# Performance work log

Hardware: AMD Instinct MI355X
Metric: run time of the kernel (lower is better)

Reference implementation:

```python
import jax, jax.numpy as jnp
import numpy as np

B, L, D = 8, 2048, 64
NEG = -1e9  # matches torch masked fill value -1000000000.0


def setup_inputs() -> dict:
    key = jax.random.key(0)
    kq, kk, kv = jax.random.split(key, 3)
    return {
        "q": jax.random.normal(kq, (B, L, D), dtype=jnp.float32),
        "k": jax.random.normal(kk, (B, L, D), dtype=jnp.float32),
        "v": jax.random.normal(kv, (B, L, D), dtype=jnp.float32),
    }


def reference(q, k, v):
    d_k = q.shape[-1]
    scale = 1.0 / np.sqrt(d_k).astype(np.float32)
    # [B, Lq, Lk] scores
    scores = jnp.einsum("bqd,bkd->bqk", q, k) * scale
    n = scores.shape[-1]
    i = jnp.arange(n)[:, None]
    j = jnp.arange(n)[None, :]
    # fw_mask: tril(diag=-1) of -1e9 -> strictly-lower entries penalized (attend to self+future)
    fw = scores + jnp.where(j < i, jnp.float32(NEG), jnp.float32(0.0))
    # bw_mask: triu(diag=1) of -1e9 -> strictly-upper entries penalized (attend to past+self)
    bw = scores + jnp.where(j > i, jnp.float32(NEG), jnp.float32(0.0))
    out = jnp.einsum("bqk,bkd->bqd", jax.nn.softmax(fw, axis=-1), v) \
        + jnp.einsum("bqk,bkd->bqd", jax.nn.softmax(bw, axis=-1), v)
    return out
```

## Files before the change

kernel.cpp:

```cpp
#include <hip/hip_runtime.h>


typedef __attribute__((ext_vector_type(8))) short short8;
typedef __attribute__((ext_vector_type(4))) float f32x4;

union Frag {
    short8 s;
    unsigned u[4];
    uint4 u4;
};

#define MFMA16(A, B, C) __builtin_amdgcn_mfma_f32_16x16x32_bf16((A), (B), (C), 0, 0, 0)

static constexpr int BB = 8, LL = 2048, DD = 64;
static constexpr float QSCALE = 0.125f * 1.44269504088896340736f;

__device__ __forceinline__ unsigned pk2(float a, float b) {
    unsigned ua = __builtin_bit_cast(unsigned, a) + 0x8000u;
    unsigned ub = __builtin_bit_cast(unsigned, b) + 0x8000u;
    return __builtin_amdgcn_perm(ub, ua, 0x07060302u);
}

__device__ __forceinline__ unsigned bperm(int addr, unsigned v) {
    return (unsigned)__builtin_amdgcn_ds_bpermute(addr, (int)v);
}

__global__ __launch_bounds__(256)
void prepack_frags(const float* __restrict__ K, const float* __restrict__ V,
                   unsigned* __restrict__ Kf, unsigned* __restrict__ Vf) {
    const int t    = threadIdx.x;
    const int lane = t & 63;
    const int col  = lane & 15;
    const int quad = lane >> 4;
    const int g    = t >> 6;
    if (blockIdx.x < 512) {
        const int b = blockIdx.x >> 6, jblk = blockIdx.x & 63, j0 = jblk << 5;
        const int f = g >> 1, h = g & 1;
        const float* src = K + ((size_t)(b * LL) + j0 + 16 * f + col) * DD + h * 32 + quad * 8;
        float4 a0 = *(const float4*)(src);
        float4 a1 = *(const float4*)(src + 4);
        uint4 o = make_uint4(pk2(a0.x, a0.y), pk2(a0.z, a0.w),
                             pk2(a1.x, a1.y), pk2(a1.z, a1.w));
        *(uint4*)(Kf + (size_t)(b * 64 + jblk) * 1024 + t * 4) = o;
    } else {
        const int idx = blockIdx.x - 512;
        const int b = idx >> 6, jblk = idx & 63, j0 = jblk << 5;
        const float* src = V + ((size_t)(b * LL) + j0 + quad * 8) * DD + 16 * g + col;
        float e[8];
        #pragma unroll
        for (int kk = 0; kk < 8; ++kk) e[kk] = src[(size_t)kk * DD];
        uint4 o = make_uint4(pk2(e[0], e[1]), pk2(e[2], e[3]),
                             pk2(e[4], e[5]), pk2(e[6], e[7]));
        *(uint4*)(Vf + (size_t)(b * 64 + jblk) * 1024 + t * 4) = o;
    }
}

__global__ __launch_bounds__(256, 3)
void attn_v3(const float* __restrict__ Q, const unsigned* __restrict__ Kf,
             const unsigned* __restrict__ Vf, float* __restrict__ O) {
    __shared__ __align__(16) float red[9216];

    const int tid  = threadIdx.x;
    const int w    = tid >> 6;
    const int lane = tid & 63;
    const int col  = lane & 15;
    const int quad = lane >> 4;

    const int b  = blockIdx.x & 7;
    const int i0 = (blockIdx.x >> 3) << 4;

    Frag qf[2];
    {
        const float* qr = Q + ((size_t)(b * LL) + i0 + col) * DD + quad * 8;
        float4 a0 = *(const float4*)(qr + 0);
        float4 a1 = *(const float4*)(qr + 4);
        float4 a2 = *(const float4*)(qr + 32);
        float4 a3 = *(const float4*)(qr + 36);
        qf[0].u[0] = pk2(a0.x * QSCALE, a0.y * QSCALE);
        qf[0].u[1] = pk2(a0.z * QSCALE, a0.w * QSCALE);
        qf[0].u[2] = pk2(a1.x * QSCALE, a1.y * QSCALE);
        qf[0].u[3] = pk2(a1.z * QSCALE, a1.w * QSCALE);
        qf[1].u[0] = pk2(a2.x * QSCALE, a2.y * QSCALE);
        qf[1].u[1] = pk2(a2.z * QSCALE, a2.w * QSCALE);
        qf[1].u[2] = pk2(a3.x * QSCALE, a3.y * QSCALE);
        qf[1].u[3] = pk2(a3.z * QSCALE, a3.w * QSCALE);
    }

    const int kbase = w << 9;
    const int dj0   = i0 & ~31;
    const unsigned* kp = Kf + (size_t)(b * 64 + (kbase >> 5)) * 1024 + lane * 4;
    const unsigned* vp = Vf + (size_t)(b * 64 + (kbase >> 5)) * 1024 + lane * 4;

    f32x4 zero = {0.f, 0.f, 0.f, 0.f};
    f32x4 ot[2][4];
    #pragma unroll
    for (int s = 0; s < 2; ++s)
        #pragma unroll
        for (int c = 0; c < 4; ++c) ot[s][c] = zero;
    float lsumF = 0.f, lsumB = 0.f;

    const int  bpA = (32 * (quad & 1) + col) << 2;
    const bool hiq = quad >= 2;

    Frag ka[4], vf[4], kan[4], vfn[4];
    #pragma unroll
    for (int g = 0; g < 4; ++g) {
        ka[g].u4 = *(const uint4*)(kp + g * 256);
        vf[g].u4 = *(const uint4*)(vp + g * 256);
    }

    for (int blk = 0; blk < 16; ++blk) {
        const int j0 = kbase + (blk << 5);
        const int no = ((blk + 1) & 15) << 10;
        #pragma unroll
        for (int g = 0; g < 4; ++g) {
            kan[g].u4 = *(const uint4*)(kp + no + g * 256);
            vfn[g].u4 = *(const uint4*)(vp + no + g * 256);
        }

        f32x4 st0 = zero, st1 = zero;
        st0 = MFMA16(ka[0].s, qf[0].s, st0);
        st0 = MFMA16(ka[1].s, qf[1].s, st0);
        st1 = MFMA16(ka[2].s, qf[0].s, st1);
        st1 = MFMA16(ka[3].s, qf[1].s, st1);

        float p0[4], p1[4];
        #pragma unroll
        for (int r = 0; r < 4; ++r) { p0[r] = exp2f(st0[r]); p1[r] = exp2f(st1[r]); }

        const bool mixed = (j0 == dj0);

        if (j0 >= dj0) {
            float m0[4], m1[4];
            if (mixed) {
                const int ig = i0 + col;
                #pragma unroll
                for (int r = 0; r < 4; ++r) {
                    const int jg = j0 + 4 * quad + r;
                    m0[r] = (jg >= ig) ? p0[r] : 0.f;
                    m1[r] = (jg + 16 >= ig) ? p1[r] : 0.f;
                }
            } else {
                #pragma unroll
                for (int r = 0; r < 4; ++r) { m0[r] = p0[r]; m1[r] = p1[r]; }
            }
            lsumF += m0[0] + m0[1] + m0[2] + m0[3] + m1[0] + m1[1] + m1[2] + m1[3];
            unsigned x01 = pk2(m0[0], m0[1]), x23 = pk2(m0[2], m0[3]);
            unsigned y01 = pk2(m1[0], m1[1]), y23 = pk2(m1[2], m1[3]);
            unsigned a0 = bperm(bpA, x01),      a1 = bperm(bpA, x23);
            unsigned a2 = bperm(bpA + 64, x01), a3 = bperm(bpA + 64, x23);
            unsigned b0 = bperm(bpA, y01),      b1 = bperm(bpA, y23);
            unsigned b2 = bperm(bpA + 64, y01), b3 = bperm(bpA + 64, y23);
            Frag pf;
            pf.u[0] = hiq ? b0 : a0;
            pf.u[1] = hiq ? b1 : a1;
            pf.u[2] = hiq ? b2 : a2;
            pf.u[3] = hiq ? b3 : a3;
            #pragma unroll
            for (int c = 0; c < 4; ++c) ot[0][c] = MFMA16(vf[c].s, pf.s, ot[0][c]);
        }
        if (j0 <= dj0) {
            float m0[4], m1[4];
            if (mixed) {
                const int ig = i0 + col;
                #pragma unroll
                for (int r = 0; r < 4; ++r) {
                    const int jg = j0 + 4 * quad + r;
                    m0[r] = (jg <= ig) ? p0[r] : 0.f;
                    m1[r] = (jg + 16 <= ig) ? p1[r] : 0.f;
                }
            } else {
                #pragma unroll
                for (int r = 0; r < 4; ++r) { m0[r] = p0[r]; m1[r] = p1[r]; }
            }
            lsumB += m0[0] + m0[1] + m0[2] + m0[3] + m1[0] + m1[1] + m1[2] + m1[3];
            unsigned x01 = pk2(m0[0], m0[1]), x23 = pk2(m0[2], m0[3]);
            unsigned y01 = pk2(m1[0], m1[1]), y23 = pk2(m1[2], m1[3]);
            unsigned a0 = bperm(bpA, x01),      a1 = bperm(bpA, x23);
            unsigned a2 = bperm(bpA + 64, x01), a3 = bperm(bpA + 64, x23);
            unsigned b0 = bperm(bpA, y01),      b1 = bperm(bpA, y23);
            unsigned b2 = bperm(bpA + 64, y01), b3 = bperm(bpA + 64, y23);
            Frag pg;
            pg.u[0] = hiq ? b0 : a0;
            pg.u[1] = hiq ? b1 : a1;
            pg.u[2] = hiq ? b2 : a2;
            pg.u[3] = hiq ? b3 : a3;
            #pragma unroll
            for (int c = 0; c < 4; ++c) ot[1][c] = MFMA16(vf[c].s, pg.s, ot[1][c]);
        }

        #pragma unroll
        for (int g = 0; g < 4; ++g) { ka[g] = kan[g]; vf[g] = vfn[g]; }
    }

    #pragma unroll
    for (int s = 0; s < 2; ++s)
        #pragma unroll
        for (int c = 0; c < 4; ++c)
            *(f32x4*)&red[((w * 2 + s) * 16 + col) * 68 + 16 * c + 4 * quad] = ot[s][c];
    red[8704 + ((w * 2 + 0) * 4 + quad) * 16 + col] = lsumF;
    red[8704 + ((w * 2 + 1) * 4 + quad) * 16 + col] = lsumB;
    __syncthreads();

    const int q  = tid >> 4;
    const int d0 = (tid & 15) << 2;
    float lf = 0.f, lb = 0.f;
    #pragma unroll
    for (int w2 = 0; w2 < 4; ++w2)
        #pragma unroll
        for (int qd = 0; qd < 4; ++qd) {
            lf += red[8704 + ((w2 * 2 + 0) * 4 + qd) * 16 + q];
            lb += red[8704 + ((w2 * 2 + 1) * 4 + qd) * 16 + q];
        }
    f32x4 aF = {0.f, 0.f, 0.f, 0.f}, aB = aF;
    #pragma unroll
    for (int w2 = 0; w2 < 4; ++w2) {
        aF += *(const f32x4*)&red[((w2 * 2 + 0) * 16 + q) * 68 + d0];
        aB += *(const f32x4*)&red[((w2 * 2 + 1) * 16 + q) * 68 + d0];
    }
    const float rf = 1.0f / lf;
    const float rb = 1.0f / lb;
    float4 o = {aF[0] * rf + aB[0] * rb, aF[1] * rf + aB[1] * rb,
                aF[2] * rf + aB[2] * rb, aF[3] * rf + aB[3] * rb};
    *(float4*)(O + ((size_t)(b * LL) + i0 + q) * DD + d0) = o;
}

__global__ __launch_bounds__(256)
void attn_fused_v1(const float* __restrict__ Q, const float* __restrict__ K,
                   const float* __restrict__ V, float* __restrict__ O) {
    __shared__ unsigned smem[8448];
    const int tid  = threadIdx.x;
    const int w    = tid >> 6;
    const int lane = tid & 63;
    const int col  = lane & 15;
    const int quad = lane >> 4;
    const int b  = blockIdx.x >> 7;
    const int i0 = (blockIdx.x & 127) << 4;
    const float* Qb = Q + (size_t)(b * LL + i0) * DD;
    const float* Kb = K + (size_t)b * LL * DD;
    const float* Vb = V + (size_t)b * LL * DD;
    unsigned* VT = smem + w * 1280;
    unsigned* Pb = smem + 5120 + w * 640;
    Frag qf[2];
    {
        const float* qr = Qb + col * DD + quad * 8;
        float4 a0 = *(const float4*)(qr + 0);
        float4 a1 = *(const float4*)(qr + 4);
        float4 a2 = *(const float4*)(qr + 32);
        float4 a3 = *(const float4*)(qr + 36);
        qf[0].u[0] = pk2(a0.x * QSCALE, a0.y * QSCALE);
        qf[0].u[1] = pk2(a0.z * QSCALE, a0.w * QSCALE);
        qf[0].u[2] = pk2(a1.x * QSCALE, a1.y * QSCALE);
        qf[0].u[3] = pk2(a1.z * QSCALE, a1.w * QSCALE);
        qf[1].u[0] = pk2(a2.x * QSCALE, a2.y * QSCALE);
        qf[1].u[1] = pk2(a2.z * QSCALE, a2.w * QSCALE);
        qf[1].u[2] = pk2(a3.x * QSCALE, a3.y * QSCALE);
        qf[1].u[3] = pk2(a3.z * QSCALE, a3.w * QSCALE);
    }
    Frag ones;
    ones.u[0] = ones.u[1] = ones.u[2] = ones.u[3] = 0x3F803F80u;
    f32x4 zero = {0.f, 0.f, 0.f, 0.f};
    f32x4 ot[2][4];
    f32x4 lacc[2];
    lacc[0] = zero; lacc[1] = zero;
    for (int s = 0; s < 2; ++s)
        for (int c = 0; c < 4; ++c) ot[s][c] = zero;
    const int kbase = w << 9;
    const int dj0   = i0 & ~31;
    for (int blk = 0; blk < 16; ++blk) {
        const int j0 = kbase + (blk << 5);
        Frag ka[2][2];
        for (int f = 0; f < 2; ++f) {
            const float* kr = Kb + (size_t)(j0 + f * 16 + col) * DD + quad * 8;
            float4 c0 = *(const float4*)(kr + 0);
            float4 c1 = *(const float4*)(kr + 4);
            float4 c2 = *(const float4*)(kr + 32);
            float4 c3 = *(const float4*)(kr + 36);
            ka[f][0].u[0] = pk2(c0.x, c0.y);
            ka[f][0].u[1] = pk2(c0.z, c0.w);
            ka[f][0].u[2] = pk2(c1.x, c1.y);
            ka[f][0].u[3] = pk2(c1.z, c1.w);
            ka[f][1].u[0] = pk2(c2.x, c2.y);
            ka[f][1].u[1] = pk2(c2.z, c2.w);
            ka[f][1].u[2] = pk2(c3.x, c3.y);
            ka[f][1].u[3] = pk2(c3.z, c3.w);
        }
        for (int u = 0; u < 4; ++u) {
            const int d0 = u * 16 + quad * 4;
            const float* va = Vb + (size_t)(j0 + 2 * col) * DD + d0;
            float4 x = *(const float4*)(va);
            float4 y = *(const float4*)(va + DD);
            VT[(d0 + 0) * 20 + col] = pk2(x.x, y.x);
            VT[(d0 + 1) * 20 + col] = pk2(x.y, y.y);
            VT[(d0 + 2) * 20 + col] = pk2(x.z, y.z);
            VT[(d0 + 3) * 20 + col] = pk2(x.w, y.w);
        }
        f32x4 st0 = zero, st1 = zero;
        st0 = MFMA16(ka[0][0].s, qf[0].s, st0);
        st0 = MFMA16(ka[0][1].s, qf[1].s, st0);
        st1 = MFMA16(ka[1][0].s, qf[0].s, st1);
        st1 = MFMA16(ka[1][1].s, qf[1].s, st1);
        float p0[4], p1[4];
        for (int r = 0; r < 4; ++r) { p0[r] = exp2f(st0[r]); p1[r] = exp2f(st1[r]); }
        bool doF, doB;
        if (j0 == dj0) {
            const int ig = i0 + col;
            unsigned* prowF = Pb + col * 20 + quad * 2;
            unsigned* prowB = prowF + 320;
            float m0[4], m1[4];
            for (int r = 0; r < 4; ++r) {
                const int jg = j0 + 4 * quad + r;
                m0[r] = (jg >= ig) ? p0[r] : 0.f;
                m1[r] = (jg + 16 >= ig) ? p1[r] : 0.f;
            }
            prowF[0] = pk2(m0[0], m0[1]);
            prowF[1] = pk2(m0[2], m0[3]);
            prowF[8] = pk2(m1[0], m1[1]);
            prowF[9] = pk2(m1[2], m1[3]);
            for (int r = 0; r < 4; ++r) {
                const int jg = j0 + 4 * quad + r;
                m0[r] = (jg <= ig) ? p0[r] : 0.f;
                m1[r] = (jg + 16 <= ig) ? p1[r] : 0.f;
            }
            prowB[0] = pk2(m0[0], m0[1]);
            prowB[1] = pk2(m0[2], m0[3]);
            prowB[8] = pk2(m1[0], m1[1]);
            prowB[9] = pk2(m1[2], m1[3]);
            doF = true; doB = true;
        } else if (j0 < i0) {
            unsigned* prowB = Pb + 320 + col * 20 + quad * 2;
            prowB[0] = pk2(p0[0], p0[1]);
            prowB[1] = pk2(p0[2], p0[3]);
            prowB[8] = pk2(p1[0], p1[1]);
            prowB[9] = pk2(p1[2], p1[3]);
            doF = false; doB = true;
        } else {
            unsigned* prowF = Pb + col * 20 + quad * 2;
            prowF[0] = pk2(p0[0], p0[1]);
            prowF[1] = pk2(p0[2], p0[3]);
            prowF[8] = pk2(p1[0], p1[1]);
            prowF[9] = pk2(p1[2], p1[3]);
            doF = true; doB = false;
        }
        Frag vfr[4];
        for (int c = 0; c < 4; ++c)
            vfr[c].u4 = *(const uint4*)(VT + (16 * c + col) * 20 + quad * 4);
        if (doF) {
            Frag pf; pf.u4 = *(const uint4*)(Pb + col * 20 + quad * 4);
            lacc[0] = MFMA16(ones.s, pf.s, lacc[0]);
            for (int c = 0; c < 4; ++c) ot[0][c] = MFMA16(vfr[c].s, pf.s, ot[0][c]);
        }
        if (doB) {
            Frag pg; pg.u4 = *(const uint4*)(Pb + 320 + col * 20 + quad * 4);
            lacc[1] = MFMA16(ones.s, pg.s, lacc[1]);
            for (int c = 0; c < 4; ++c) ot[1][c] = MFMA16(vfr[c].s, pg.s, ot[1][c]);
        }
    }
    __syncthreads();
    float* red  = (float*)smem;
    float* lred = (float*)(smem + 8192);
    for (int s = 0; s < 2; ++s)
        for (int c = 0; c < 4; ++c)
            for (int r = 0; r < 4; ++r)
                red[((w * 2 + s) * 64 + 16 * c + 4 * quad + r) * 16 + col] = ot[s][c][r];
    if (lane < 16) {
        lred[(w * 2 + 0) * 16 + col] = lacc[0][0];
        lred[(w * 2 + 1) * 16 + col] = lacc[1][0];
    }
    __syncthreads();
    const int ri = tid >> 4;
    const int db = (tid & 15) << 2;
    float lf = 0.f, lb = 0.f;
    for (int w2 = 0; w2 < 4; ++w2) {
        lf += lred[(w2 * 2 + 0) * 16 + ri];
        lb += lred[(w2 * 2 + 1) * 16 + ri];
    }
    const float rf = 1.0f / lf;
    const float rb = 1.0f / lb;
    float acc[4];
    for (int kk = 0; kk < 4; ++kk) {
        float af = 0.f, ab = 0.f;
        for (int w2 = 0; w2 < 4; ++w2) {
            af += red[((w2 * 2 + 0) * 64 + db + kk) * 16 + ri];
            ab += red[((w2 * 2 + 1) * 64 + db + kk) * 16 + ri];
        }
        acc[kk] = af * rf + ab * rb;
    }
    float4 o = {acc[0], acc[1], acc[2], acc[3]};
    *(float4*)(O + (size_t)(b * LL + i0 + ri) * DD + db) = o;
}

extern "C" void kernel_launch(void* const* d_in, const int* in_sizes, int n_in,
                              void* d_out, int out_size, void* d_ws, size_t ws_size,
                              hipStream_t stream) {
    const float* q = (const float*)d_in[0];
    const float* k = (const float*)d_in[1];
    const float* v = (const float*)d_in[2];
    float* o = (float*)d_out;
    (void)in_sizes; (void)n_in; (void)out_size;

    const size_t WS_NEED = (size_t)2 * BB * 64 * 1024 * 4 * sizeof(unsigned);
    if (ws_size >= WS_NEED) {
        unsigned* Kf = (unsigned*)d_ws;
        unsigned* Vf = Kf + (size_t)BB * 64 * 1024;
        prepack_frags<<<dim3(1024), dim3(256), 0, stream>>>(k, v, Kf, Vf);
        attn_v3<<<dim3(1024), dim3(256), 0, stream>>>(q, Kf, Vf, o);
    } else {
        attn_fused_v1<<<dim3(BB * (LL / 16)), dim3(256), 0, stream>>>(q, k, v, o);
    }
}
```

Measured before the change: 87.24 us.

## Process 32 query rows per block to reuse K/V fragments across two query tiles

Each block now handles two 16-row query tiles, so every loaded K and V fragment feeds twice as many MFMAs, and the grid is halved to 512 blocks. The KV loop is manually unrolled by two with ping-pong fragment buffers instead of copying next-to-current registers each iteration. The aim is to halve global K/V fragment traffic per unit of work. The cost is more registers, doubled shared memory for the reduction, launch bounds lowered to 2 blocks per SM, and fewer blocks to spread across CUs.

```diff
diff --git a/kernel.cpp b/kernel.cpp
--- a/kernel.cpp
+++ b/kernel.cpp
@@ -55,10 +55,10 @@
     }
 }
 
-__global__ __launch_bounds__(256, 3)
-void attn_v3(const float* __restrict__ Q, const unsigned* __restrict__ Kf,
+__global__ __launch_bounds__(256, 2)
+void attn_v4(const float* __restrict__ Q, const unsigned* __restrict__ Kf,
              const unsigned* __restrict__ Vf, float* __restrict__ O) {
-    __shared__ __align__(16) float red[9216];
+    __shared__ __align__(16) float red[18432];
 
     const int tid  = threadIdx.x;
     const int w    = tid >> 6;
@@ -67,162 +67,197 @@
     const int quad = lane >> 4;
 
     const int b  = blockIdx.x & 7;
-    const int i0 = (blockIdx.x >> 3) << 4;
-
-    Frag qf[2];
+    const int i0 = (blockIdx.x >> 3) << 5;
+
+    Frag qf[2][2];
     {
         const float* qr = Q + ((size_t)(b * LL) + i0 + col) * DD + quad * 8;
-        float4 a0 = *(const float4*)(qr + 0);
-        float4 a1 = *(const float4*)(qr + 4);
-        float4 a2 = *(const float4*)(qr + 32);
-        float4 a3 = *(const float4*)(qr + 36);
-        qf[0].u[0] = pk2(a0.x * QSCALE, a0.y * QSCALE);
-        qf[0].u[1] = pk2(a0.z * QSCALE, a0.w * QSCALE);
-        qf[0].u[2] = pk2(a1.x * QSCALE, a1.y * QSCALE);
-        qf[0].u[3] = pk2(a1.z * QSCALE, a1.w * QSCALE);
-        qf[1].u[0] = pk2(a2.x * QSCALE, a2.y * QSCALE);
-        qf[1].u[1] = pk2(a2.z * QSCALE, a2.w * QSCALE);
-        qf[1].u[2] = pk2(a3.x * QSCALE, a3.y * QSCALE);
-        qf[1].u[3] = pk2(a3.z * QSCALE, a3.w * QSCALE);
+        #pragma unroll
+        for (int qt = 0; qt < 2; ++qt) {
+            const float* qp = qr + (size_t)qt * 16 * DD;
+            float4 a0 = *(const float4*)(qp + 0);
+            float4 a1 = *(const float4*)(qp + 4);
+            float4 a2 = *(const float4*)(qp + 32);
+            float4 a3 = *(const float4*)(qp + 36);
+            qf[qt][0].u[0] = pk2(a0.x * QSCALE, a0.y * QSCALE);
+            qf[qt][0].u[1] = pk2(a0.z * QSCALE, a0.w * QSCALE);
+            qf[qt][0].u[2] = pk2(a1.x * QSCALE, a1.y * QSCALE);
+            qf[qt][0].u[3] = pk2(a1.z * QSCALE, a1.w * QSCALE);
+            qf[qt][1].u[0] = pk2(a2.x * QSCALE, a2.y * QSCALE);
+            qf[qt][1].u[1] = pk2(a2.z * QSCALE, a2.w * QSCALE);
+            qf[qt][1].u[2] = pk2(a3.x * QSCALE, a3.y * QSCALE);
+            qf[qt][1].u[3] = pk2(a3.z * QSCALE, a3.w * QSCALE);
+        }
     }
 
     const int kbase = w << 9;
-    const int dj0   = i0 & ~31;
     const unsigned* kp = Kf + (size_t)(b * 64 + (kbase >> 5)) * 1024 + lane * 4;
     const unsigned* vp = Vf + (size_t)(b * 64 + (kbase >> 5)) * 1024 + lane * 4;
 
     f32x4 zero = {0.f, 0.f, 0.f, 0.f};
-    f32x4 ot[2][4];
+    f32x4 ot[2][2][4];
     #pragma unroll
     for (int s = 0; s < 2; ++s)
         #pragma unroll
-        for (int c = 0; c < 4; ++c) ot[s][c] = zero;
-    float lsumF = 0.f, lsumB = 0.f;
+        for (int qt = 0; qt < 2; ++qt)
+            #pragma unroll
+            for (int c = 0; c < 4; ++c) ot[s][qt][c] = zero;
+    float lsF[2] = {0.f, 0.f}, lsB[2] = {0.f, 0.f};
 
     const int  bpA = (32 * (quad & 1) + col) << 2;
     const bool hiq = quad >= 2;
 
-    Frag ka[4], vf[4], kan[4], vfn[4];
+    Frag kaA[4], vfA[4], kaB[4], vfB[4];
     #pragma unroll
     for (int g = 0; g < 4; ++g) {
-        ka[g].u4 = *(const uint4*)(kp + g * 256);
-        vf[g].u4 = *(const uint4*)(vp + g * 256);
-    }
-
-    for (int blk = 0; blk < 16; ++blk) {
+        kaA[g].u4 = *(const uint4*)(kp + g * 256);
+        vfA[g].u4 = *(const uint4*)(vp + g * 256);
+    }
+
+    auto body = [&](Frag (&ck)[4], Frag (&cv)[4], Frag (&nk)[4], Frag (&nv)[4],
+                    const int blk) {
         const int j0 = kbase + (blk << 5);
         const int no = ((blk + 1) & 15) << 10;
         #pragma unroll
         for (int g = 0; g < 4; ++g) {
-            kan[g].u4 = *(const uint4*)(kp + no + g * 256);
-            vfn[g].u4 = *(const uint4*)(vp + no + g * 256);
-        }
-
-        f32x4 st0 = zero, st1 = zero;
-        st0 = MFMA16(ka[0].s, qf[0].s, st0);
-        st0 = MFMA16(ka[1].s, qf[1].s, st0);
-        st1 = MFMA16(ka[2].s, qf[0].s, st1);
-        st1 = MFMA16(ka[3].s, qf[1].s, st1);
-
-        float p0[4], p1[4];
-        #pragma unroll
-        for (int r = 0; r < 4; ++r) { p0[r] = exp2f(st0[r]); p1[r] = exp2f(st1[r]); }
-
-        const bool mixed = (j0 == dj0);
-
-        if (j0 >= dj0) {
-            float m0[4], m1[4];
-            if (mixed) {
-                const int ig = i0 + col;
+            nk[g].u4 = *(const uint4*)(kp + no + g * 256);
+            nv[g].u4 = *(const uint4*)(vp + no + g * 256);
+        }
+
+        f32x4 st00 = zero, st01 = zero, st10 = zero, st11 = zero;
+        st00 = MFMA16(ck[0].s, qf[0][0].s, st00);
+        st00 = MFMA16(ck[1].s, qf[0][1].s, st00);
+        st01 = MFMA16(ck[0].s, qf[1][0].s, st01);
+        st01 = MFMA16(ck[1].s, qf[1][1].s, st01);
+        st10 = MFMA16(ck[2].s, qf[0][0].s, st10);
+        st10 = MFMA16(ck[3].s, qf[0][1].s, st10);
+        st11 = MFMA16(ck[2].s, qf[1][0].s, st11);
+        st11 = MFMA16(ck[3].s, qf[1][1].s, st11);
+
+        float p0[2][4], p1[2][4];
+        #pragma unroll
+        for (int r = 0; r < 4; ++r) {
+            p0[0][r] = exp2f(st00[r]);
+            p0[1][r] = exp2f(st01[r]);
+            p1[0][r] = exp2f(st10[r]);
+            p1[1][r] = exp2f(st11[r]);
+        }
+
+        const bool mixed = (j0 == i0);
+
+        if (j0 >= i0) {
+            #pragma unroll
+            for (int qt = 0; qt < 2; ++qt) {
+                float m0[4], m1[4];
+                if (mixed) {
+                    const int ig = i0 + 16 * qt + col;
+                    #pragma unroll
+                    for (int r = 0; r < 4; ++r) {
+                        const int jg = j0 + 4 * quad + r;
+                        m0[r] = (jg >= ig) ? p0[qt][r] : 0.f;
+                        m1[r] = (jg + 16 >= ig) ? p1[qt][r] : 0.f;
+                    }
+                } else {
+                    #pragma unroll
+                    for (int r = 0; r < 4; ++r) { m0[r] = p0[qt][r]; m1[r] = p1[qt][r]; }
+                }
+                lsF[qt] += m0[0] + m0[1] + m0[2] + m0[3] + m1[0] + m1[1] + m1[2] + m1[3];
+                unsigned x01 = pk2(m0[0], m0[1]), x23 = pk2(m0[2], m0[3]);
+                unsigned y01 = pk2(m1[0], m1[1]), y23 = pk2(m1[2], m1[3]);
+                unsigned a0 = bperm(bpA, x01),      a1 = bperm(bpA, x23);
+                unsigned a2 = bperm(bpA + 64, x01), a3 = bperm(bpA + 64, x23);
+                unsigned b0 = bperm(bpA, y01),      b1 = bperm(bpA, y23);
+                unsigned b2 = bperm(bpA + 64, y01), b3 = bperm(bpA + 64, y23);
+                Frag pf;
+                pf.u[0] = hiq ? b0 : a0;
+                pf.u[1] = hiq ? b1 : a1;
+                pf.u[2] = hiq ? b2 : a2;
+                pf.u[3] = hiq ? b3 : a3;
                 #pragma unroll
-                for (int r = 0; r < 4; ++r) {
-                    const int jg = j0 + 4 * quad + r;
-                    m0[r] = (jg >= ig) ? p0[r] : 0.f;
-                    m1[r] = (jg + 16 >= ig) ? p1[r] : 0.f;
+                for (int c = 0; c < 4; ++c)
+                    ot[0][qt][c] = MFMA16(cv[c].s, pf.s, ot[0][qt][c]);
+            }
+        }
+        if (j0 <= i0) {
+            #pragma unroll
+            for (int qt = 0; qt < 2; ++qt) {
+                float m0[4], m1[4];
+                if (mixed) {
+                    const int ig = i0 + 16 * qt + col;
+                    #pragma unroll
+                    for (int r = 0; r < 4; ++r) {
+                        const int jg = j0 + 4 * quad + r;
+                        m0[r] = (jg <= ig) ? p0[qt][r] : 0.f;
+                        m1[r] = (jg + 16 <= ig) ? p1[qt][r] : 0.f;
+                    }
+                } else {
+                    #pragma unroll
+                    for (int r = 0; r < 4; ++r) { m0[r] = p0[qt][r]; m1[r] = p1[qt][r]; }
                 }
-            } else {
+                lsB[qt] += m0[0] + m0[1] + m0[2] + m0[3] + m1[0] + m1[1] + m1[2] + m1[3];
+                unsigned x01 = pk2(m0[0], m0[1]), x23 = pk2(m0[2], m0[3]);
+                unsigned y01 = pk2(m1[0], m1[1]), y23 = pk2(m1[2], m1[3]);
+                unsigned a0 = bperm(bpA, x01),      a1 = bperm(bpA, x23);
+                unsigned a2 = bperm(bpA + 64, x01), a3 = bperm(bpA + 64, x23);
+                unsigned b0 = bperm(bpA, y01),      b1 = bperm(bpA, y23);
+                unsigned b2 = bperm(bpA + 64, y01), b3 = bperm(bpA + 64, y23);
+                Frag pg;
+                pg.u[0] = hiq ? b0 : a0;
+                pg.u[1] = hiq ? b1 : a1;
+                pg.u[2] = hiq ? b2 : a2;
+                pg.u[3] = hiq ? b3 : a3;
                 #pragma unroll
-                for (int r = 0; r < 4; ++r) { m0[r] = p0[r]; m1[r] = p1[r]; }
+                for (int c = 0; c < 4; ++c)
+                    ot[1][qt][c] = MFMA16(cv[c].s, pg.s, ot[1][qt][c]);
             }
-            lsumF += m0[0] + m0[1] + m0[2] + m0[3] + m1[0] + m1[1] + m1[2] + m1[3];
-            unsigned x01 = pk2(m0[0], m0[1]), x23 = pk2(m0[2], m0[3]);
-            unsigned y01 = pk2(m1[0], m1[1]), y23 = pk2(m1[2], m1[3]);
-            unsigned a0 = bperm(bpA, x01),      a1 = bperm(bpA, x23);
-            unsigned a2 = bperm(bpA + 64, x01), a3 = bperm(bpA + 64, x23);
-            unsigned b0 = bperm(bpA, y01),      b1 = bperm(bpA, y23);
-            unsigned b2 = bperm(bpA + 64, y01), b3 = bperm(bpA + 64, y23);
-            Frag pf;
-            pf.u[0] = hiq ? b0 : a0;
-            pf.u[1] = hiq ? b1 : a1;
-            pf.u[2] = hiq ? b2 : a2;
-            pf.u[3] = hiq ? b3 : a3;
-            #pragma unroll
-            for (int c = 0; c < 4; ++c) ot[0][c] = MFMA16(vf[c].s, pf.s, ot[0][c]);
-        }
-        if (j0 <= dj0) {
-            float m0[4], m1[4];
-            if (mixed) {
-                const int ig = i0 + col;
-                #pragma unroll
-                for (int r = 0; r < 4; ++r) {
-                    const int jg = j0 + 4 * quad + r;
-                    m0[r] = (jg <= ig) ? p0[r] : 0.f;
-                    m1[r] = (jg + 16 <= ig) ? p1[r] : 0.f;
-                }
-            } else {
-                #pragma unroll
-                for (int r = 0; r < 4; ++r) { m0[r] = p0[r]; m1[r] = p1[r]; }
-            }
-            lsumB += m0[0] + m0[1] + m0[2] + m0[3] + m1[0] + m1[1] + m1[2] + m1[3];
-            unsigned x01 = pk2(m0[0], m0[1]), x23 = pk2(m0[2], m0[3]);
-            unsigned y01 = pk2(m1[0], m1[1]), y23 = pk2(m1[2], m1[3]);
-            unsigned a0 = bperm(bpA, x01),      a1 = bperm(bpA, x23);
-            unsigned a2 = bperm(bpA + 64, x01), a3 = bperm(bpA + 64, x23);
-            unsigned b0 = bperm(bpA, y01),      b1 = bperm(bpA, y23);
-            unsigned b2 = bperm(bpA + 64, y01), b3 = bperm(bpA + 64, y23);
-            Frag pg;
-            pg.u[0] = hiq ? b0 : a0;
-            pg.u[1] = hiq ? b1 : a1;
-            pg.u[2] = hiq ? b2 : a2;
-            pg.u[3] = hiq ? b3 : a3;
-            #pragma unroll
-            for (int c = 0; c < 4; ++c) ot[1][c] = MFMA16(vf[c].s, pg.s, ot[1][c]);
-        }
-
-        #pragma unroll
-        for (int g = 0; g < 4; ++g) { ka[g] = kan[g]; vf[g] = vfn[g]; }
+        }
+    };
+
+    for (int it = 0; it < 8; ++it) {
+        body(kaA, vfA, kaB, vfB, 2 * it);
+        body(kaB, vfB, kaA, vfA, 2 * it + 1);
     }
 
     #pragma unroll
     for (int s = 0; s < 2; ++s)
         #pragma unroll
-        for (int c = 0; c < 4; ++c)
-            *(f32x4*)&red[((w * 2 + s) * 16 + col) * 68 + 16 * c + 4 * quad] = ot[s][c];
-    red[8704 + ((w * 2 + 0) * 4 + quad) * 16 + col] = lsumF;
-    red[8704 + ((w * 2 + 1) * 4 + quad) * 16 + col] = lsumB;
+        for (int qt = 0; qt < 2; ++qt)
+            #pragma unroll
+            for (int c = 0; c < 4; ++c)
+                *(f32x4*)&red[((w * 2 + s) * 32 + qt * 16 + col) * 68 + 16 * c + 4 * quad] =
+                    ot[s][qt][c];
+    #pragma unroll
+    for (int qt = 0; qt < 2; ++qt) {
+        red[17408 + (((w * 2 + 0) * 2 + qt) * 4 + quad) * 16 + col] = lsF[qt];
+        red[17408 + (((w * 2 + 1) * 2 + qt) * 4 + quad) * 16 + col] = lsB[qt];
+    }
     __syncthreads();
 
     const int q  = tid >> 4;
     const int d0 = (tid & 15) << 2;
-    float lf = 0.f, lb = 0.f;
     #pragma unroll
-    for (int w2 = 0; w2 < 4; ++w2)
-        #pragma unroll
-        for (int qd = 0; qd < 4; ++qd) {
-            lf += red[8704 + ((w2 * 2 + 0) * 4 + qd) * 16 + q];
-            lb += red[8704 + ((w2 * 2 + 1) * 4 + qd) * 16 + q];
-        }
-    f32x4 aF = {0.f, 0.f, 0.f, 0.f}, aB = aF;
-    #pragma unroll
-    for (int w2 = 0; w2 < 4; ++w2) {
-        aF += *(const f32x4*)&red[((w2 * 2 + 0) * 16 + q) * 68 + d0];
-        aB += *(const f32x4*)&red[((w2 * 2 + 1) * 16 + q) * 68 + d0];
-    }
-    const float rf = 1.0f / lf;
-    const float rb = 1.0f / lb;
-    float4 o = {aF[0] * rf + aB[0] * rb, aF[1] * rf + aB[1] * rb,
-                aF[2] * rf + aB[2] * rb, aF[3] * rf + aB[3] * rb};
-    *(float4*)(O + ((size_t)(b * LL) + i0 + q) * DD + d0) = o;
+    for (int qh = 0; qh < 2; ++qh) {
+        const int qq = qh * 16 + q;
+        float lf = 0.f, lb = 0.f;
+        #pragma unroll
+        for (int w2 = 0; w2 < 4; ++w2)
+            #pragma unroll
+            for (int qd = 0; qd < 4; ++qd) {
+                lf += red[17408 + (((w2 * 2 + 0) * 2 + qh) * 4 + qd) * 16 + q];
+                lb += red[17408 + (((w2 * 2 + 1) * 2 + qh) * 4 + qd) * 16 + q];
+            }
+        f32x4 aF = {0.f, 0.f, 0.f, 0.f}, aB = aF;
+        #pragma unroll
+        for (int w2 = 0; w2 < 4; ++w2) {
+            aF += *(const f32x4*)&red[((w2 * 2 + 0) * 32 + qq) * 68 + d0];
+            aB += *(const f32x4*)&red[((w2 * 2 + 1) * 32 + qq) * 68 + d0];
+        }
+        const float rf = 1.0f / lf;
+        const float rb = 1.0f / lb;
+        float4 o = {aF[0] * rf + aB[0] * rb, aF[1] * rf + aB[1] * rb,
+                    aF[2] * rf + aB[2] * rb, aF[3] * rf + aB[3] * rb};
+        *(float4*)(O + ((size_t)(b * LL) + i0 + qq) * DD + d0) = o;
+    }
 }
 
 __global__ __launch_bounds__(256)
@@ -404,7 +439,7 @@
         unsigned* Kf = (unsigned*)d_ws;
         unsigned* Vf = Kf + (size_t)BB * 64 * 1024;
         prepack_frags<<<dim3(1024), dim3(256), 0, stream>>>(k, v, Kf, Vf);
-        attn_v3<<<dim3(1024), dim3(256), 0, stream>>>(q, Kf, Vf, o);
+        attn_v4<<<dim3(512), dim3(256), 0, stream>>>(q, Kf, Vf, o);
     } else {
         attn_fused_v1<<<dim3(BB * (LL / 16)), dim3(256), 0, stream>>>(q, k, v, o);
     }
```

Result: faster. 84.36 us (-3.3%).
